# Optimization experiments

Hardware: AMD Instinct MI355X
Metric: run time of the kernel (lower is better)

Reference implementation:

```python
import jax, jax.numpy as jnp
import numpy as np

N_SRC = 50000; N_DST = 50000; E = 800000
IN_NODE = 128; IN_EDGE = 16; OUT_NODE = 64; OUT_EDGE = 16; H = 4
LEAKY_SLOPE = 0.01  # F.leaky_relu default used inside dgl EGATConv


def setup_inputs() -> dict:
    key = jax.random.key(0)
    ks = jax.random.split(key, 11)
    return dict(
        nfeats=jax.random.normal(ks[0], (N_SRC, IN_NODE), jnp.float32),
        dst_feats=jax.random.normal(ks[1], (N_DST, IN_NODE), jnp.float32),
        reward=jax.random.uniform(ks[2], (E,), jnp.float32),
        src=jax.random.randint(ks[3], (E,), 0, N_SRC),
        dst=jax.random.randint(ks[4], (E,), 0, N_DST),
        W_ns=jax.random.normal(ks[5], (IN_NODE, H * OUT_NODE), jnp.float32) * 0.05,
        b_ns=jnp.zeros((H * OUT_NODE,), jnp.float32),
        W_ni=jax.random.normal(ks[6], (IN_NODE, H * OUT_EDGE), jnp.float32) * 0.05,
        W_nj=jax.random.normal(ks[7], (IN_NODE, H * OUT_EDGE), jnp.float32) * 0.05,
        W_fij=jax.random.normal(ks[8], (IN_EDGE, H * OUT_EDGE), jnp.float32) * 0.05,
        attn=jax.random.normal(ks[9], (H, OUT_EDGE), jnp.float32) * 0.05,
        b_e=jnp.zeros((H * OUT_EDGE,), jnp.float32),
    )


def reference(nfeats, dst_feats, reward, src, dst,
              W_ns, b_ns, W_ni, W_nj, W_fij, attn, b_e):
    # EGAT.forward with num_layers=1: efeats = reward repeated to IN_EDGE cols
    efeats = jnp.repeat(reward[:, None], IN_EDGE, axis=1)              # (E, Fe_in)
    # --- EGATConv ---
    f_ni = nfeats @ W_ni                                               # (Ns, H*Fe)
    f_nj = dst_feats @ W_nj                                            # (Nd, H*Fe)
    f_out = f_ni[src] + f_nj[dst] + efeats @ W_fij + b_e               # (E, H*Fe)
    f_out = jax.nn.leaky_relu(f_out, LEAKY_SLOPE).reshape(E, H, OUT_EDGE)
    e = jnp.einsum('ehf,hf->eh', f_out, attn)                          # (E, H)
    # edge softmax over incoming edges of each dst node (stable)
    m = jax.ops.segment_max(e, dst, num_segments=N_DST)                # (Nd, H)
    a = jnp.exp(e - m[dst])
    s = jax.ops.segment_sum(a, dst, num_segments=N_DST)                # (Nd, H)
    a = a / jnp.where(s > 0, s, 1.0)[dst]                              # (E, H)
    # weighted aggregation of projected src features
    h_src = (nfeats @ W_ns + b_ns).reshape(N_SRC, H, OUT_NODE)
    msg = h_src[src] * a[:, :, None]                                   # (E, H, Fn)
    h_out = jax.ops.segment_sum(msg, dst, num_segments=N_DST)          # (Nd, H, Fn)
    # wrapper: mean over heads then ReLU
    return jax.nn.relu(h_out.mean(axis=1))                             # (Nd, Fn)
```

## Files before the change

### kernel.cpp

```cpp
#include <hip/hip_runtime.h>

#define IN_NODE 128
#define OUT_NODE 64
#define NHEAD 4
#define HN 256
#define HE 64
#define LEAKY 0.01f
#define MAXD 96

typedef __attribute__((ext_vector_type(8))) short bf16x8;
typedef __attribute__((ext_vector_type(4))) float f32x4;

__device__ __forceinline__ float bf2f(unsigned short u) {
    union { unsigned u; float f; } v; v.u = ((unsigned)u) << 16; return v.f;
}
__device__ __forceinline__ unsigned short f2bf(float x) {
    union { float f; unsigned u; } v; v.f = x;
    unsigned r = v.u + 0x7FFF + ((v.u >> 16) & 1);
    return (unsigned short)(r >> 16);
}
__device__ __forceinline__ bf16x8 cvt8(float4 a, float4 b) {
    bf16x8 r;
    r[0] = (short)f2bf(a.x); r[1] = (short)f2bf(a.y);
    r[2] = (short)f2bf(a.z); r[3] = (short)f2bf(a.w);
    r[4] = (short)f2bf(b.x); r[5] = (short)f2bf(b.y);
    r[6] = (short)f2bf(b.z); r[7] = (short)f2bf(b.w);
    return r;
}

__global__ void prep_hist(const float* __restrict__ W_fij,
                          const float* __restrict__ W_ni,
                          const float* __restrict__ W_ns,
                          const float* __restrict__ W_nj,
                          const int* __restrict__ dst,
                          float* __restrict__ wsum, unsigned short* __restrict__ WT,
                          int* __restrict__ cnt, int E) {
    int b = blockIdx.x;
    if (b == 0) {
        int k = threadIdx.x;
        if (k < 64) {
            float s = 0.f;
#pragma unroll
            for (int c = 0; c < 16; ++c) s += W_fij[c * 64 + k];
            wsum[k] = s;
        }
        return;
    }
    if (b <= 12) {
        int base = (b - 1) * 4096 + threadIdx.x;
#pragma unroll
        for (int i = 0; i < 16; ++i) {
            int idx = base + i * 256;
            int g   = idx >> 11;
            int rem = idx & 2047;
            int c   = rem >> 9;
            int l   = (rem >> 3) & 63;
            int j   = rem & 7;
            int nl  = l & 15;
            int k   = c * 32 + (l >> 4) * 8 + j;
            unsigned short v;
            if (g < 4)       v = f2bf(W_ni[k * 64  + g * 16 + nl]);
            else if (g < 20) v = f2bf(W_ns[k * 256 + (g - 4) * 16 + nl]);
            else             v = f2bf(W_nj[k * 64  + (g - 20) * 16 + nl]);
            WT[idx] = v;
        }
        return;
    }
    int i = (b - 13) * 256 + threadIdx.x;
    if (i < E) atomicAdd(&cnt[dst[i]], 1);
}

__global__ __launch_bounds__(256) void scan_all(const int* __restrict__ cnt,
                                                int* __restrict__ row_ptr,
                                                int* __restrict__ partials,
                                                int* __restrict__ flags,
                                                int n, int E, int nb) {
    __shared__ int sums[256];
    __shared__ int s_base;
    int tid = threadIdx.x, b = blockIdx.x;
    int base = b * 1024;
    int v[4]; int tsum = 0;
#pragma unroll
    for (int j = 0; j < 4; ++j) {
        int idx = base + tid * 4 + j;
        v[j] = (idx < n) ? cnt[idx] : 0;
        tsum += v[j];
    }
    sums[tid] = tsum;
    __syncthreads();
    for (int off = 1; off < 256; off <<= 1) {
        int x = (tid >= off) ? sums[tid - off] : 0;
        __syncthreads();
        sums[tid] += x;
        __syncthreads();
    }
    if (tid == 255) {
        __hip_atomic_store(&partials[b], sums[255], __ATOMIC_RELAXED, __HIP_MEMORY_SCOPE_AGENT);
        __hip_atomic_store(&flags[b], 1, __ATOMIC_RELEASE, __HIP_MEMORY_SCOPE_AGENT);
    }
    if (tid < 64) {
        int val = 0;
        if (tid < nb) {
            while (__hip_atomic_load(&flags[tid], __ATOMIC_ACQUIRE, __HIP_MEMORY_SCOPE_AGENT) == 0) {
                __builtin_amdgcn_s_sleep(1);
            }
            val = __hip_atomic_load(&partials[tid], __ATOMIC_RELAXED, __HIP_MEMORY_SCOPE_AGENT);
        }
#pragma unroll
        for (int o = 1; o < 64; o <<= 1) {
            int x = __shfl_up(val, o);
            if (tid >= o) val += x;
        }
        int off = (b > 0) ? __shfl(val, b - 1) : 0;
        if (tid == 0) s_base = off;
    }
    __syncthreads();
    int run = s_base + sums[tid] - tsum;
#pragma unroll
    for (int j = 0; j < 4; ++j) {
        int idx = base + tid * 4 + j;
        if (idx < n) row_ptr[idx] = run;
        run += v[j];
    }
    if (b == nb - 1 && tid == 0) row_ptr[n] = E;
}

template<int NG, int G0>
__device__ __forceinline__ void gemm_tile(
    const float* __restrict__ A, int rowBase, int M,
    const unsigned short* __restrict__ WB, const float* __restrict__ b_ns,
    unsigned short* __restrict__ f_ni, unsigned short* __restrict__ h_src,
    unsigned short* __restrict__ f_nj, unsigned short* As)
{
    const int t = threadIdx.x;
    const float4* A4 = reinterpret_cast<const float4*>(A);
#pragma unroll
    for (int j = 0; j < 4; ++j) {
        int gi = j * 256 + t;
        int r  = gi >> 4;
        int gr = rowBase + r; if (gr >= M) gr = M - 1;
        int fi = (gi & 15) * 2;
        float4 a0 = A4[(size_t)gr * 32 + fi];
        float4 a1 = A4[(size_t)gr * 32 + fi + 1];
        int byteoff = (gi * 16) ^ ((r & 7) << 4);
        *reinterpret_cast<bf16x8*>(reinterpret_cast<char*>(As) + byteoff) = cvt8(a0, a1);
    }
    __syncthreads();

    const int lane = t & 63, w = t >> 6;
    const int rw = rowBase + w * 16;
    if (rw >= M) return;
    const int m = lane & 15, q = lane >> 4;
    const int tr = w * 16 + m;

    f32x4 acc[NG] = {};
    const char* Asb = reinterpret_cast<const char*>(As);
#pragma unroll
    for (int c = 0; c < 4; ++c) {
        int gi  = tr * 16 + c * 4 + q;
        int off = (gi * 16) ^ ((tr & 7) << 4);
        bf16x8 af = *reinterpret_cast<const bf16x8*>(Asb + off);
#pragma unroll
        for (int g = 0; g < NG; ++g) {
            bf16x8 bf = *reinterpret_cast<const bf16x8*>(
                WB + (size_t)(((G0 + g) * 4 + c) * 64 + lane) * 8);
            acc[g] = __builtin_amdgcn_mfma_f32_16x16x32_bf16(af, bf, acc[g], 0, 0, 0);
        }
    }

#pragma unroll
    for (int g = 0; g < NG; ++g) {
        const int ga = G0 + g;
        unsigned short* C; int N, colBase; const float* bias = nullptr;
        if (ga < 4)       { C = f_ni;  N = 64;  colBase = ga * 16; }
        else if (ga < 20) { C = h_src; N = 256; colBase = (ga - 4) * 16; bias = b_ns; }
        else              { C = f_nj;  N = 64;  colBase = (ga - 20) * 16; }
        int col = colBase + m;
        float bv = bias ? bias[col] : 0.f;
#pragma unroll
        for (int rr = 0; rr < 4; ++rr) {
            int orow = rw + q * 4 + rr;
            if (orow < M) C[(size_t)orow * N + col] = f2bf(acc[g][rr] + bv);
        }
    }
}

__global__ __launch_bounds__(256) void mega(
    const float* __restrict__ nfeats, const float* __restrict__ dst_feats,
    const unsigned short* __restrict__ WT, const float* __restrict__ b_ns,
    const int* __restrict__ src, const int* __restrict__ dst,
    const float* __restrict__ reward, const int* __restrict__ row_ptr,
    int* __restrict__ cnt,
    unsigned short* __restrict__ f_ni, unsigned short* __restrict__ h_src,
    unsigned short* __restrict__ f_nj, int2* __restrict__ sr_s,
    int Ns, int Nd, int E, int nBlkNf, int nBlkDj, int nScatter)
{
    __shared__ __align__(16) unsigned short As[64 * 128];
    const int g = blockIdx.x / 3, r = blockIdx.x % 3;
    if (r == 0) {
        if (g < nBlkNf) {
            gemm_tile<20, 0>(nfeats, g * 64, Ns, WT, b_ns, f_ni, h_src, f_nj, As);
        } else if (g < nBlkNf + nBlkDj) {
            gemm_tile<4, 20>(dst_feats, (g - nBlkNf) * 64, Nd, WT, b_ns, f_ni, h_src, f_nj, As);
        }
        return;
    }
    const int sb = g * 2 + (r - 1);
    if (sb >= nScatter) return;
    int i = sb * 256 + threadIdx.x;
    if (i >= E) return;
    int d = dst[i];
    int pos = row_ptr[d] + atomicSub(&cnt[d], 1) - 1;
    sr_s[pos] = make_int2(src[i], __float_as_int(reward[i]));
}

__global__ __launch_bounds__(256) void fused_agg(
    const unsigned short* __restrict__ f_ni, const unsigned short* __restrict__ f_nj,
    const unsigned short* __restrict__ h_src, const int2* __restrict__ sr_s,
    const int* __restrict__ row_ptr,
    const float* __restrict__ wsum, const float* __restrict__ b_e,
    const float* __restrict__ attn, float* __restrict__ out, int Nd)
{
    __shared__ float s_e[4][MAXD][4];
    __shared__ int   s_sn[4][MAXD];
    const int wv = threadIdx.x >> 6, lane = threadIdx.x & 63;
    const int d = blockIdx.x * 4 + wv;
    if (d >= Nd) return;
    const int l = lane & 15, sub = lane >> 4;
    const int beg = row_ptr[d];
    const int end = row_ptr[d + 1];

    for (int i = lane; i < MAXD; i += 64) s_sn[wv][i] = -1;

    ushort4 uj = *reinterpret_cast<const ushort4*>(f_nj + (size_t)d * HE + 4 * l);
    float4 fnj = { bf2f(uj.x), bf2f(uj.y), bf2f(uj.z), bf2f(uj.w) };
    float4 ws = *reinterpret_cast<const float4*>(wsum + 4 * l);
    float4 be = *reinterpret_cast<const float4*>(b_e + 4 * l);
    float4 at = *reinterpret_cast<const float4*>(attn + 4 * l);

    float den = 0.f;
    for (int base = beg; base < end; base += 4) {
        int slot = base + sub;
        if (slot < end) {
            int2 sr = sr_s[slot];
            int sn = sr.x;
            float r = __int_as_float(sr.y);
            ushort4 ui = *reinterpret_cast<const ushort4*>(f_ni + (size_t)sn * HE + 4 * l);
            float t, v;
            v = bf2f(ui.x) + fnj.x + r * ws.x + be.x; v = (v >= 0.f) ? v : LEAKY * v; t  = v * at.x;
            v = bf2f(ui.y) + fnj.y + r * ws.y + be.y; v = (v >= 0.f) ? v : LEAKY * v; t += v * at.y;
            v = bf2f(ui.z) + fnj.z + r * ws.z + be.z; v = (v >= 0.f) ? v : LEAKY * v; t += v * at.z;
            v = bf2f(ui.w) + fnj.w + r * ws.w + be.w; v = (v >= 0.f) ? v : LEAKY * v; t += v * at.w;
            t += __shfl_xor(t, 1);
            t += __shfl_xor(t, 2);
            float ev = __expf(t);
            den += ev;
            int idx = slot - beg;
            if (idx < MAXD) {
                if ((l & 3) == 0) s_e[wv][idx][l >> 2] = ev;
                if (l == 0) s_sn[wv][idx] = sn;
            }
        }
    }
    den += __shfl_xor(den, 16);
    den += __shfl_xor(den, 32);
    float dh = __shfl(den, (lane >> 4) << 2);
    float invh = (dh > 0.f) ? 1.f / dh : 0.f;
    const int h = lane >> 4;

    float a0 = 0.f, a1 = 0.f, a2 = 0.f, a3 = 0.f;
    int cap = min(end - beg, MAXD);
    int npad = (cap + 7) & ~7;
    for (int idx0 = 0; idx0 < npad; idx0 += 8) {
#pragma unroll
        for (int j = 0; j < 8; ++j) {
            int idx = idx0 + j;
            int sn = s_sn[wv][idx];
            float wgt = (sn >= 0) ? s_e[wv][idx][h] * invh : 0.f;
            int sa = (sn >= 0) ? sn : 0;
            ushort4 u = *reinterpret_cast<const ushort4*>(h_src + (size_t)sa * HN + lane * 4);
            a0 = fmaf(wgt, bf2f(u.x), a0);
            a1 = fmaf(wgt, bf2f(u.y), a1);
            a2 = fmaf(wgt, bf2f(u.z), a2);
            a3 = fmaf(wgt, bf2f(u.w), a3);
        }
    }
    for (int slot = beg + MAXD; slot < end; ++slot) {
        int2 sr = sr_s[slot];
        int sn = sr.x;
        float r = __int_as_float(sr.y);
        float v = bf2f(f_ni[(size_t)sn * HE + lane]) + bf2f(f_nj[(size_t)d * HE + lane])
                + r * wsum[lane] + b_e[lane];
        v = (v >= 0.f) ? v : LEAKY * v;
        float t = v * attn[lane];
        t += __shfl_xor(t, 1);
        t += __shfl_xor(t, 2);
        t += __shfl_xor(t, 4);
        t += __shfl_xor(t, 8);
        float wgt = __expf(t) * invh;
        ushort4 u = *reinterpret_cast<const ushort4*>(h_src + (size_t)sn * HN + lane * 4);
        a0 = fmaf(wgt, bf2f(u.x), a0);
        a1 = fmaf(wgt, bf2f(u.y), a1);
        a2 = fmaf(wgt, bf2f(u.z), a2);
        a3 = fmaf(wgt, bf2f(u.w), a3);
    }

    a0 += __shfl_xor(a0, 16); a0 += __shfl_xor(a0, 32);
    a1 += __shfl_xor(a1, 16); a1 += __shfl_xor(a1, 32);
    a2 += __shfl_xor(a2, 16); a2 += __shfl_xor(a2, 32);
    a3 += __shfl_xor(a3, 16); a3 += __shfl_xor(a3, 32);
    if (lane < 16) {
        float4 o = { fmaxf(a0 * 0.25f, 0.f), fmaxf(a1 * 0.25f, 0.f),
                     fmaxf(a2 * 0.25f, 0.f), fmaxf(a3 * 0.25f, 0.f) };
        *reinterpret_cast<float4*>(out + (size_t)d * OUT_NODE + lane * 4) = o;
    }
}

static inline char* align256(char* p) {
    return (char*)(((uintptr_t)p + 255) & ~(uintptr_t)255);
}

extern "C" void kernel_launch(void* const* d_in, const int* in_sizes, int n_in,
                              void* d_out, int out_size, void* d_ws, size_t ws_size,
                              hipStream_t stream) {
    const float* nfeats    = (const float*)d_in[0];
    const float* dst_feats = (const float*)d_in[1];
    const float* reward    = (const float*)d_in[2];
    const int*   src       = (const int*)d_in[3];
    const int*   dst       = (const int*)d_in[4];
    const float* W_ns      = (const float*)d_in[5];
    const float* b_ns      = (const float*)d_in[6];
    const float* W_ni      = (const float*)d_in[7];
    const float* W_nj      = (const float*)d_in[8];
    const float* W_fij     = (const float*)d_in[9];
    const float* attn      = (const float*)d_in[10];
    const float* b_e       = (const float*)d_in[11];
    float* out = (float*)d_out;

    const int Ns = in_sizes[0] / IN_NODE;
    const int Nd = in_sizes[1] / IN_NODE;
    const int E  = in_sizes[2];

    char* ws = (char*)d_ws;
    unsigned short* f_ni  = (unsigned short*)ws; ws = align256(ws + (size_t)Ns * HE * 2);
    unsigned short* f_nj  = (unsigned short*)ws; ws = align256(ws + (size_t)Nd * HE * 2);
    unsigned short* h_src = (unsigned short*)ws; ws = align256(ws + (size_t)Ns * HN * 2);
    unsigned short* WT    = (unsigned short*)ws; ws = align256(ws + 49152 * 2);
    float* wsum    = (float*)ws; ws = align256(ws + HE * 4);
    int*   cnt     = (int*)ws;
    int*   flags   = cnt + Nd;   ws = align256(ws + (size_t)(Nd + 64) * 4);
    int*   row_ptr = (int*)ws;   ws = align256(ws + (size_t)(Nd + 1) * 4);
    int*   partials= (int*)ws;   ws = align256(ws + 256 * 4);
    int2*  sr_s    = (int2*)ws;  ws = align256(ws + (size_t)E * 8);

    hipMemsetAsync(cnt, 0, (size_t)(Nd + 64) * 4, stream);

    prep_hist<<<13 + (E + 255) / 256, 256, 0, stream>>>(
        W_fij, W_ni, W_ns, W_nj, dst, wsum, WT, cnt, E);

    int nb = (Nd + 1023) / 1024;
    scan_all<<<nb, 256, 0, stream>>>(cnt, row_ptr, partials, flags, Nd, E, nb);

    int nBlkNf = (Ns + 63) / 64;
    int nBlkDj = (Nd + 63) / 64;
    int nG = nBlkNf + nBlkDj;
    int nScatter = (E + 255) / 256;
    int nGroups = (nG > (nScatter + 1) / 2) ? nG : (nScatter + 1) / 2;
    mega<<<nGroups * 3, 256, 0, stream>>>(
        nfeats, dst_feats, WT, b_ns, src, dst, reward, row_ptr, cnt,
        f_ni, h_src, f_nj, sr_s, Ns, Nd, E, nBlkNf, nBlkDj, nScatter);

    fused_agg<<<(Nd + 3) / 4, 256, 0, stream>>>(
        f_ni, f_nj, h_src, sr_s, row_ptr, wsum, b_e, attn, out, Nd);
}
```

Baseline: 282.7 us.

## Fuse softmax score and weighted aggregation into one pass over edges

Merges the two-phase aggregation, which stored per-edge exp scores and source ids in LDS and then re-read them, into a single loop. Weights and source ids are broadcast across the wave with shuffles, and normalisation by the denominator is applied once at the end. This drops the LDS staging, the padding to multiples of 8 and the separate high-degree fallback path, at the cost of less independent gather work in flight per iteration (4 edges instead of 8).

```diff
diff --git a/kernel.cpp b/kernel.cpp
--- a/kernel.cpp
+++ b/kernel.cpp
@@ -6,7 +6,6 @@
 #define HN 256
 #define HE 64
 #define LEAKY 0.01f
-#define MAXD 96
 
 typedef __attribute__((ext_vector_type(8))) short bf16x8;
 typedef __attribute__((ext_vector_type(4))) float f32x4;
@@ -221,16 +220,13 @@
     const float* __restrict__ wsum, const float* __restrict__ b_e,
     const float* __restrict__ attn, float* __restrict__ out, int Nd)
 {
-    __shared__ float s_e[4][MAXD][4];
-    __shared__ int   s_sn[4][MAXD];
     const int wv = threadIdx.x >> 6, lane = threadIdx.x & 63;
     const int d = blockIdx.x * 4 + wv;
     if (d >= Nd) return;
     const int l = lane & 15, sub = lane >> 4;
     const int beg = row_ptr[d];
     const int end = row_ptr[d + 1];
-
-    for (int i = lane; i < MAXD; i += 64) s_sn[wv][i] = -1;
+    const int hsel = (lane >> 4) << 2;
 
     ushort4 uj = *reinterpret_cast<const ushort4*>(f_nj + (size_t)d * HE + 4 * l);
     float4 fnj = { bf2f(uj.x), bf2f(uj.y), bf2f(uj.z), bf2f(uj.w) };
@@ -239,11 +235,45 @@
     float4 at = *reinterpret_cast<const float4*>(attn + 4 * l);
 
     float den = 0.f;
-    for (int base = beg; base < end; base += 4) {
+    float a0 = 0.f, a1 = 0.f, a2 = 0.f, a3 = 0.f;
+
+    const int deg = end - beg;
+    const int nfull = deg & ~3;
+
+    for (int base = beg; base < beg + nfull; base += 4) {
+        int2 sr = sr_s[base + sub];
+        int sn = sr.x;
+        float r = __int_as_float(sr.y);
+        ushort4 ui = *reinterpret_cast<const ushort4*>(f_ni + (size_t)sn * HE + 4 * l);
+        float t, v;
+        v = bf2f(ui.x) + fnj.x + r * ws.x + be.x; v = (v >= 0.f) ? v : LEAKY * v; t  = v * at.x;
+        v = bf2f(ui.y) + fnj.y + r * ws.y + be.y; v = (v >= 0.f) ? v : LEAKY * v; t += v * at.y;
+        v = bf2f(ui.z) + fnj.z + r * ws.z + be.z; v = (v >= 0.f) ? v : LEAKY * v; t += v * at.z;
+        v = bf2f(ui.w) + fnj.w + r * ws.w + be.w; v = (v >= 0.f) ? v : LEAKY * v; t += v * at.w;
+        t += __shfl_xor(t, 1);
+        t += __shfl_xor(t, 2);
+        float ev = __expf(t);
+        den += ev;
+#pragma unroll
+        for (int e = 0; e < 4; ++e) {
+            float w  = __shfl(ev, e * 16 + hsel);
+            int   sa = __shfl(sn, e * 16);
+            ushort4 u = *reinterpret_cast<const ushort4*>(h_src + (size_t)sa * HN + lane * 4);
+            a0 = fmaf(w, bf2f(u.x), a0);
+            a1 = fmaf(w, bf2f(u.y), a1);
+            a2 = fmaf(w, bf2f(u.z), a2);
+            a3 = fmaf(w, bf2f(u.w), a3);
+        }
+    }
+
+    const int rem = deg & 3;
+    if (rem) {
+        int base = beg + nfull;
         int slot = base + sub;
-        if (slot < end) {
+        float ev = 0.f; int sn = 0;
+        if (sub < rem) {
             int2 sr = sr_s[slot];
-            int sn = sr.x;
+            sn = sr.x;
             float r = __int_as_float(sr.y);
             ushort4 ui = *reinterpret_cast<const ushort4*>(f_ni + (size_t)sn * HE + 4 * l);
             float t, v;
@@ -253,57 +283,25 @@
             v = bf2f(ui.w) + fnj.w + r * ws.w + be.w; v = (v >= 0.f) ? v : LEAKY * v; t += v * at.w;
             t += __shfl_xor(t, 1);
             t += __shfl_xor(t, 2);
-            float ev = __expf(t);
+            ev = __expf(t);
             den += ev;
-            int idx = slot - beg;
-            if (idx < MAXD) {
-                if ((l & 3) == 0) s_e[wv][idx][l >> 2] = ev;
-                if (l == 0) s_sn[wv][idx] = sn;
-            }
-        }
-    }
+        }
+        for (int e = 0; e < rem; ++e) {
+            float w  = __shfl(ev, e * 16 + hsel);
+            int   sa = __shfl(sn, e * 16);
+            ushort4 u = *reinterpret_cast<const ushort4*>(h_src + (size_t)sa * HN + lane * 4);
+            a0 = fmaf(w, bf2f(u.x), a0);
+            a1 = fmaf(w, bf2f(u.y), a1);
+            a2 = fmaf(w, bf2f(u.z), a2);
+            a3 = fmaf(w, bf2f(u.w), a3);
+        }
+    }
+
     den += __shfl_xor(den, 16);
     den += __shfl_xor(den, 32);
-    float dh = __shfl(den, (lane >> 4) << 2);
+    float dh = __shfl(den, hsel);
     float invh = (dh > 0.f) ? 1.f / dh : 0.f;
-    const int h = lane >> 4;
-
-    float a0 = 0.f, a1 = 0.f, a2 = 0.f, a3 = 0.f;
-    int cap = min(end - beg, MAXD);
-    int npad = (cap + 7) & ~7;
-    for (int idx0 = 0; idx0 < npad; idx0 += 8) {
-#pragma unroll
-        for (int j = 0; j < 8; ++j) {
-            int idx = idx0 + j;
-            int sn = s_sn[wv][idx];
-            float wgt = (sn >= 0) ? s_e[wv][idx][h] * invh : 0.f;
-            int sa = (sn >= 0) ? sn : 0;
-            ushort4 u = *reinterpret_cast<const ushort4*>(h_src + (size_t)sa * HN + lane * 4);
-            a0 = fmaf(wgt, bf2f(u.x), a0);
-            a1 = fmaf(wgt, bf2f(u.y), a1);
-            a2 = fmaf(wgt, bf2f(u.z), a2);
-            a3 = fmaf(wgt, bf2f(u.w), a3);
-        }
-    }
-    for (int slot = beg + MAXD; slot < end; ++slot) {
-        int2 sr = sr_s[slot];
-        int sn = sr.x;
-        float r = __int_as_float(sr.y);
-        float v = bf2f(f_ni[(size_t)sn * HE + lane]) + bf2f(f_nj[(size_t)d * HE + lane])
-                + r * wsum[lane] + b_e[lane];
-        v = (v >= 0.f) ? v : LEAKY * v;
-        float t = v * attn[lane];
-        t += __shfl_xor(t, 1);
-        t += __shfl_xor(t, 2);
-        t += __shfl_xor(t, 4);
-        t += __shfl_xor(t, 8);
-        float wgt = __expf(t) * invh;
-        ushort4 u = *reinterpret_cast<const ushort4*>(h_src + (size_t)sn * HN + lane * 4);
-        a0 = fmaf(wgt, bf2f(u.x), a0);
-        a1 = fmaf(wgt, bf2f(u.y), a1);
-        a2 = fmaf(wgt, bf2f(u.z), a2);
-        a3 = fmaf(wgt, bf2f(u.w), a3);
-    }
+    a0 *= invh; a1 *= invh; a2 *= invh; a3 *= invh;
 
     a0 += __shfl_xor(a0, 16); a0 += __shfl_xor(a0, 32);
     a1 += __shfl_xor(a1, 16); a1 += __shfl_xor(a1, 32);
```

New measurement: 278.1 us. Within noise of the previous version (-1.6%).
